# Optimization experiments

Hardware: AMD Instinct MI355X
Metric: run time of the kernel (lower is better)

## Reference

```python
import jax, jax.numpy as jnp
import numpy as np

N = 50000       # nodes
E = 800000      # edges (before self-loops)
F_IN = 128
HID = 64
HEADS = 4
OUT_DIM = 128
N_CLS = 2
NG = 500        # num graphs
SLOPE = 0.2     # GATConv leaky_relu negative slope
EPS = 1e-5      # BatchNorm eps


def setup_inputs() -> dict:
    key = jax.random.key(0)
    ks = jax.random.split(key, 24)
    s = 0.05
    d = {
        "x": jax.random.normal(ks[0], (N, F_IN), jnp.float32),
        "edge_index": jax.random.randint(ks[1], (2, E), 0, N, jnp.int64),
        "batch": jnp.sort(jax.random.randint(ks[2], (N,), 0, NG, jnp.int64)),
        # GATConv 1
        "W1": jax.random.normal(ks[3], (F_IN, HEADS * HID), jnp.float32) * s,
        "att_src1": jax.random.normal(ks[4], (HEADS, HID), jnp.float32) * s,
        "att_dst1": jax.random.normal(ks[5], (HEADS, HID), jnp.float32) * s,
        "b1": jnp.zeros((HEADS * HID,), jnp.float32),
        # BN1 (eval mode)
        "g1": jnp.ones((HEADS * HID,), jnp.float32),
        "be1": jnp.zeros((HEADS * HID,), jnp.float32),
        "rm1": jnp.zeros((HEADS * HID,), jnp.float32),
        "rv1": jnp.ones((HEADS * HID,), jnp.float32),
        # GATConv 2
        "W2": jax.random.normal(ks[6], (HEADS * HID, HEADS * HID), jnp.float32) * s,
        "att_src2": jax.random.normal(ks[7], (HEADS, HID), jnp.float32) * s,
        "att_dst2": jax.random.normal(ks[8], (HEADS, HID), jnp.float32) * s,
        "b2": jnp.zeros((HEADS * HID,), jnp.float32),
        # BN2 (eval mode)
        "g2": jnp.ones((HEADS * HID,), jnp.float32),
        "be2": jnp.zeros((HEADS * HID,), jnp.float32),
        "rm2": jnp.zeros((HEADS * HID,), jnp.float32),
        "rv2": jnp.ones((HEADS * HID,), jnp.float32),
        # MLP head
        "lw1": jax.random.normal(ks[9], (HEADS * HID, OUT_DIM), jnp.float32) * s,
        "lb1": jnp.zeros((OUT_DIM,), jnp.float32),
        "lw2": jax.random.normal(ks[10], (OUT_DIM, N_CLS), jnp.float32) * s,
        "lb2": jnp.zeros((N_CLS,), jnp.float32),
    }
    return d


def _gat_conv(x, src, dst, W, a_src, a_dst, b):
    """PyG GATConv (concat heads, add_self_loops=True, eval -> no dropout)."""
    n = x.shape[0]
    h = (x @ W).reshape(n, HEADS, -1)            # [N, H, C]
    loop = jnp.arange(n)
    s = jnp.concatenate([src, loop])             # self-loops appended
    d = jnp.concatenate([dst, loop])
    a_s = jnp.sum(h * a_src, axis=-1)            # [N, H]
    a_d = jnp.sum(h * a_dst, axis=-1)            # [N, H]
    e = jax.nn.leaky_relu(a_s[s] + a_d[d], SLOPE)   # [Et, H]
    # softmax over incoming edges per destination node
    m = jax.ops.segment_max(e, d, num_segments=n)
    ex = jnp.exp(e - m[d])
    denom = jax.ops.segment_sum(ex, d, num_segments=n)
    alpha = ex / denom[d]                        # [Et, H]
    msg = h[s] * alpha[:, :, None]               # [Et, H, C]
    out = jax.ops.segment_sum(msg, d, num_segments=n)
    return out.reshape(n, -1) + b


def _bn_eval(x, g, be, rm, rv):
    return (x - rm) * jax.lax.rsqrt(rv + EPS) * g + be


def reference(x, edge_index, batch, W1, att_src1, att_dst1, b1, g1, be1, rm1, rv1,
              W2, att_src2, att_dst2, b2, g2, be2, rm2, rv2, lw1, lb1, lw2, lb2):
    src, dst = edge_index[0], edge_index[1]
    h = jax.nn.relu(_gat_conv(x, src, dst, W1, att_src1, att_dst1, b1))
    h = _bn_eval(h, g1, be1, rm1, rv1)
    h = jax.nn.relu(_gat_conv(h, src, dst, W2, att_src2, att_dst2, b2))
    h = _bn_eval(h, g2, be2, rm2, rv2)
    # global mean pool over graphs
    sums = jax.ops.segment_sum(h, batch, num_segments=NG)
    cnt = jax.ops.segment_sum(jnp.ones((h.shape[0],), h.dtype), batch, num_segments=NG)
    pooled = sums / jnp.clip(cnt, 1.0)[:, None]
    z = jax.nn.relu(pooled @ lw1 + lb1)
    return z @ lw2 + lb2
```

## Files before the change

### kernel.cpp

```cpp
#include <hip/hip_runtime.h>
#include <hip/hip_bf16.h>
#include <math.h>

#define N_NODES 50000
#define M_PAD   50048
#define TILE_M  64
#define NBLK_GEMM (M_PAD / TILE_M)
#define N_EDGES 800000
#define F_IN 128
#define HID 64
#define HEADS 4
#define FEAT 256
#define OUT_DIM 128
#define N_CLS 2
#define NG 500
#define SLOPE 0.2f
#define BN_EPS 1e-5f
#define ECAP 64
#define ET (N_EDGES + N_NODES)
#define EH ((ET + 1) / 2)
#define NBLK_BUILD ((EH + 255) / 256)

#define XCONV (N_NODES * F_IN / 8)
#define XPAD_ULL ((M_PAD - N_NODES) * F_IN / 4)
#define HPAD_ULL ((M_PAD - N_NODES) * FEAT / 4)
#define PREP_THREADS (XCONV + F_IN * 256 + FEAT * 256 + XPAD_ULL + HPAD_ULL)
#define NBLK_PREP ((PREP_THREADS + 255) / 256)

typedef __attribute__((ext_vector_type(8))) short short8;
typedef __attribute__((ext_vector_type(4))) float floatx4;
typedef __attribute__((ext_vector_type(2))) float floatx2;

__device__ inline unsigned short f2bf(float f) {
    unsigned int u = __float_as_uint(f);
    unsigned int lsb = (u >> 16) & 1u;
    return (unsigned short)((u + 0x7fffu + lsb) >> 16);
}

__global__ __launch_bounds__(256) void prep_build(
    const float* __restrict__ x, const float* __restrict__ W1,
    const float* __restrict__ W2,
    unsigned short* __restrict__ xbf, unsigned short* __restrict__ W1T,
    unsigned short* __restrict__ W2T, unsigned short* __restrict__ h1bf,
    const int* __restrict__ src, const int* __restrict__ dst,
    int* __restrict__ deg, unsigned short* __restrict__ ell,
    int* __restrict__ ovf_cnt, int* __restrict__ ovf) {
    int b = blockIdx.x;
    int t = threadIdx.x;
    if (b < NBLK_PREP) {
        int gid = b * 256 + t;
        if (gid < XCONV) {
            const float4* xp = (const float4*)&x[gid * 8];
            float4 f0 = xp[0], f1 = xp[1];
            uint4 pk;
            pk.x = (unsigned)f2bf(f0.x) | ((unsigned)f2bf(f0.y) << 16);
            pk.y = (unsigned)f2bf(f0.z) | ((unsigned)f2bf(f0.w) << 16);
            pk.z = (unsigned)f2bf(f1.x) | ((unsigned)f2bf(f1.y) << 16);
            pk.w = (unsigned)f2bf(f1.z) | ((unsigned)f2bf(f1.w) << 16);
            *(uint4*)&xbf[gid * 8] = pk;
            return;
        }
        int j = gid - XCONV;
        if (j < F_IN * 256) {
            int k = j >> 8, n = j & 255;
            W1T[n * F_IN + k] = f2bf(W1[j]);
            return;
        }
        j -= F_IN * 256;
        if (j < FEAT * 256) {
            int k = j >> 8, n = j & 255;
            W2T[n * FEAT + k] = f2bf(W2[j]);
            return;
        }
        j -= FEAT * 256;
        if (j < XPAD_ULL) {
            ((unsigned long long*)(xbf + (size_t)N_NODES * F_IN))[j] = 0ULL;
            return;
        }
        j -= XPAD_ULL;
        if (j < HPAD_ULL) {
            ((unsigned long long*)(h1bf + (size_t)N_NODES * FEAT))[j] = 0ULL;
        }
        return;
    }
    int i = (b - NBLK_PREP) * 256 + t;
    if (i >= EH) return;
    int ss[2], dd[2], pp[2];
    int nv = 0;
    #pragma unroll
    for (int j = 0; j < 2; j++) {
        int e = i + j * EH;
        if (e < ET) {
            if (e < N_EDGES) { ss[nv] = src[e]; dd[nv] = dst[e]; }
            else             { ss[nv] = dd[nv] = e - N_EDGES; }
            nv++;
        }
    }
    #pragma unroll
    for (int j = 0; j < 2; j++)
        if (j < nv) pp[j] = atomicAdd(&deg[dd[j]], 1);
    #pragma unroll
    for (int j = 0; j < 2; j++) {
        if (j >= nv) continue;
        if (pp[j] < ECAP) {
            ell[dd[j] * ECAP + pp[j]] = (unsigned short)ss[j];
        } else {
            int k = atomicAdd(ovf_cnt, 1);
            ovf[2 * k] = ss[j];
            ovf[2 * k + 1] = dd[j];
        }
    }
}

template<int K>
__global__ __launch_bounds__(256, 4) void gemm_mfma(
    const unsigned short* __restrict__ Ab, const unsigned short* __restrict__ BT,
    const float* __restrict__ att_src, const float* __restrict__ att_dst,
    unsigned char* __restrict__ h8, float* __restrict__ a_s,
    float* __restrict__ a_d) {
    constexpr int LS = 40;
    constexpr int C8 = 272;
    __shared__ __align__(16) unsigned char smem_raw[(TILE_M + FEAT) * LS * 2];
    int t = threadIdx.x;

    unsigned short* As = (unsigned short*)smem_raw;
    unsigned short* Bs = As + TILE_M * LS;
    unsigned char*  s8 = smem_raw;
    int lane = t & 63, w = t >> 6;
    int row0 = blockIdx.x * TILE_M;
    int mrow = lane & 15, quad = lane >> 4;

    floatx4 acc[4][4] = {};

    int rA = t >> 2, cA = (t & 3) * 8;

    for (int k0 = 0; k0 < K; k0 += 32) {
        *(uint4*)&As[rA * LS + cA] =
            *(const uint4*)&Ab[(long long)(row0 + rA) * K + k0 + cA];
        #pragma unroll
        for (int j = 0; j < 4; j++) {
            int r = rA + j * 64;
            *(uint4*)&Bs[r * LS + cA] = *(const uint4*)&BT[(long long)r * K + k0 + cA];
        }
        __syncthreads();
        short8 bf[4];
        #pragma unroll
        for (int ni = 0; ni < 4; ni++)
            bf[ni] = *(const short8*)&Bs[(w * 64 + ni * 16 + mrow) * LS + quad * 8];
        #pragma unroll
        for (int mi = 0; mi < 4; mi++) {
            short8 af = *(const short8*)&As[(mi * 16 + mrow) * LS + quad * 8];
            #pragma unroll
            for (int ni = 0; ni < 4; ni++)
                acc[mi][ni] = __builtin_amdgcn_mfma_f32_16x16x32_bf16(af, bf[ni],
                                                                      acc[mi][ni], 0, 0, 0);
        }
        __syncthreads();
    }

    float ats[4], atd[4];
    #pragma unroll
    for (int ni = 0; ni < 4; ni++) {
        ats[ni] = att_src[w * 64 + ni * 16 + mrow];
        atd[ni] = att_dst[w * 64 + ni * 16 + mrow];
    }
    #pragma unroll
    for (int mi = 0; mi < 4; mi++) {
        #pragma unroll
        for (int r = 0; r < 4; r++) {
            int row = row0 + mi * 16 + quad * 4 + r;
            float ps = 0.f, pd = 0.f;
            #pragma unroll
            for (int ni = 0; ni < 4; ni++) {
                float v = acc[mi][ni][r];
                ps += v * ats[ni];
                pd += v * atd[ni];
            }
            #pragma unroll
            for (int off = 1; off < 16; off <<= 1) {
                ps += __shfl_xor(ps, off);
                pd += __shfl_xor(pd, off);
            }
            if (mrow == 0 && row < N_NODES) {
                a_s[row * 4 + w] = ps;
                a_d[row * 4 + w] = pd;
            }
        }
    }

    #pragma unroll
    for (int mi = 0; mi < 4; mi++)
        #pragma unroll
        for (int r = 0; r < 4; r++) {
            int row = mi * 16 + quad * 4 + r;
            #pragma unroll
            for (int ni = 0; ni < 4; ni += 2) {
                int pk = __builtin_amdgcn_cvt_pk_fp8_f32(acc[mi][ni][r],
                                                         acc[mi][ni + 1][r], 0, false);
                s8[row * C8 + w * 64 + ni * 16 + mrow]       = (unsigned char)(pk & 0xff);
                s8[row * C8 + w * 64 + (ni + 1) * 16 + mrow] = (unsigned char)((pk >> 8) & 0xff);
            }
        }
    __syncthreads();
    {
        int r2 = t >> 2, q = t & 3;
        const uint4* sp = (const uint4*)&s8[r2 * C8 + q * 64];
        uint4* dp = (uint4*)&h8[(long long)(row0 + r2) * FEAT + q * 64];
        #pragma unroll
        for (int k = 0; k < 4; k++)
            dp[k] = sp[k];
    }
}

__global__ __launch_bounds__(256) void gat_fused(
    const int* __restrict__ deg_arr, const unsigned short* __restrict__ ell,
    const int* __restrict__ ovf_cnt, const int* __restrict__ ovf,
    const float* __restrict__ a_s, const float* __restrict__ a_d,
    const unsigned char* __restrict__ h8, const float* __restrict__ bias,
    const float* __restrict__ g, const float* __restrict__ be,
    const float* __restrict__ rm, const float* __restrict__ rv,
    unsigned short* __restrict__ out16) {
    int t = threadIdx.x;
    int lane = t & 63;
    int w = t >> 6;
    int hd = lane >> 4;
    int d = blockIdx.x * 4 + w;

    __shared__ float p_lds[4 * ECAP * 4];
    __shared__ int   o_lds[4 * ECAP];
    float* pw = &p_lds[w * ECAP * 4];
    int*   ow = &o_lds[w * ECAP];

    const unsigned int* __restrict__ H1 = (const unsigned int*)h8;

    int deg = deg_arr[d];
    float4 ad4 = *(const float4*)&a_d[d * 4];

    float den = 0.f;
    float4 acc = make_float4(0.f, 0.f, 0.f, 0.f);

    if (deg <= ECAP) {
        float lg[4] = {-INFINITY, -INFINITY, -INFINITY, -INFINITY};
        if (lane < deg) {
            int s = ell[d * ECAP + lane];
            ow[lane] = s * 64;
            float4 as4 = *(const float4*)&a_s[s * 4];
            float e0 = as4.x + ad4.x; lg[0] = e0 > 0.f ? e0 : SLOPE * e0;
            float e1 = as4.y + ad4.y; lg[1] = e1 > 0.f ? e1 : SLOPE * e1;
            float e2 = as4.z + ad4.z; lg[2] = e2 > 0.f ? e2 : SLOPE * e2;
            float e3 = as4.w + ad4.w; lg[3] = e3 > 0.f ? e3 : SLOPE * e3;
        }
        float mm = fmaxf(fmaxf(lg[0], lg[1]), fmaxf(lg[2], lg[3]));
        #pragma unroll
        for (int off = 1; off < 64; off <<= 1) mm = fmaxf(mm, __shfl_xor(mm, off));
        if (lane < deg) {
            float4 pq;
            pq.x = __expf(lg[0] - mm);
            pq.y = __expf(lg[1] - mm);
            pq.z = __expf(lg[2] - mm);
            pq.w = __expf(lg[3] - mm);
            *(float4*)&pw[lane * 4] = pq;
        }
        int e = 0;
        for (; e + 1 < deg; e += 2) {
            int oA = ow[e], oB = ow[e + 1];
            float pA = pw[e * 4 + hd], pB = pw[(e + 1) * 4 + hd];
            int uA = (int)H1[oA + lane];
            int uB = (int)H1[oB + lane];
            den += pA + pB;
            floatx2 a0 = __builtin_amdgcn_cvt_pk_f32_fp8(uA, false);
            floatx2 a1 = __builtin_amdgcn_cvt_pk_f32_fp8(uA, true);
            floatx2 b0 = __builtin_amdgcn_cvt_pk_f32_fp8(uB, false);
            floatx2 b1 = __builtin_amdgcn_cvt_pk_f32_fp8(uB, true);
            acc.x += pA * a0.x; acc.y += pA * a0.y;
            acc.z += pA * a1.x; acc.w += pA * a1.y;
            acc.x += pB * b0.x; acc.y += pB * b0.y;
            acc.z += pB * b1.x; acc.w += pB * b1.y;
        }
        if (e < deg) {
            int oA = ow[e];
            float pA = pw[e * 4 + hd];
            int uA = (int)H1[oA + lane];
            den += pA;
            floatx2 a0 = __builtin_amdgcn_cvt_pk_f32_fp8(uA, false);
            floatx2 a1 = __builtin_amdgcn_cvt_pk_f32_fp8(uA, true);
            acc.x += pA * a0.x; acc.y += pA * a0.y;
            acc.z += pA * a1.x; acc.w += pA * a1.y;
        }
    } else {
        float m_old;
        {
            int s = ell[d * ECAP + lane];
            ow[lane] = s * 64;
            float4 as4 = *(const float4*)&a_s[s * 4];
            float lg[4];
            float e0 = as4.x + ad4.x; lg[0] = e0 > 0.f ? e0 : SLOPE * e0;
            float e1 = as4.y + ad4.y; lg[1] = e1 > 0.f ? e1 : SLOPE * e1;
            float e2 = as4.z + ad4.z; lg[2] = e2 > 0.f ? e2 : SLOPE * e2;
            float e3 = as4.w + ad4.w; lg[3] = e3 > 0.f ? e3 : SLOPE * e3;
            float mm = fmaxf(fmaxf(lg[0], lg[1]), fmaxf(lg[2], lg[3]));
            #pragma unroll
            for (int off = 1; off < 64; off <<= 1) mm = fmaxf(mm, __shfl_xor(mm, off));
            m_old = mm;
            float4 pq;
            pq.x = __expf(lg[0] - mm);
            pq.y = __expf(lg[1] - mm);
            pq.z = __expf(lg[2] - mm);
            pq.w = __expf(lg[3] - mm);
            *(float4*)&pw[lane * 4] = pq;
            for (int e = 0; e < ECAP; e++) {
                int oA = ow[e];
                float pA = pw[e * 4 + hd];
                int uA = (int)H1[oA + lane];
                den += pA;
                floatx2 a0 = __builtin_amdgcn_cvt_pk_f32_fp8(uA, false);
                floatx2 a1 = __builtin_amdgcn_cvt_pk_f32_fp8(uA, true);
                acc.x += pA * a0.x; acc.y += pA * a0.y;
                acc.z += pA * a1.x; acc.w += pA * a1.y;
            }
        }
        int nov = *ovf_cnt;
        for (int i = 0; i < nov; i++) {
            int s2 = ovf[2 * i], d2 = ovf[2 * i + 1];
            if (d2 != d) continue;
            float4 as4 = *(const float4*)&a_s[s2 * 4];
            float lg[4];
            float e0 = as4.x + ad4.x; lg[0] = e0 > 0.f ? e0 : SLOPE * e0;
            float e1 = as4.y + ad4.y; lg[1] = e1 > 0.f ? e1 : SLOPE * e1;
            float e2 = as4.z + ad4.z; lg[2] = e2 > 0.f ? e2 : SLOPE * e2;
            float e3 = as4.w + ad4.w; lg[3] = e3 > 0.f ? e3 : SLOPE * e3;
            float mmax = fmaxf(fmaxf(lg[0], lg[1]), fmaxf(lg[2], lg[3]));
            float m_new = fmaxf(m_old, mmax);
            float alpha = __expf(m_old - m_new);
            m_old = m_new;
            float ph = __expf(lg[hd] - m_new);
            acc.x *= alpha; acc.y *= alpha; acc.z *= alpha; acc.w *= alpha;
            den = den * alpha + ph;
            int u = (int)H1[s2 * 64 + lane];
            floatx2 a0 = __builtin_amdgcn_cvt_pk_f32_fp8(u, false);
            floatx2 a1 = __builtin_amdgcn_cvt_pk_f32_fp8(u, true);
            acc.x += ph * a0.x; acc.y += ph * a0.y;
            acc.z += ph * a1.x; acc.w += ph * a1.y;
        }
    }
    float inv = 1.f / den;
    int c0 = lane * 4;
    float4 bi = *(const float4*)&bias[c0];
    float4 gg = *(const float4*)&g[c0];
    float4 bb = *(const float4*)&be[c0];
    float4 mm4 = *(const float4*)&rm[c0];
    float4 vv = *(const float4*)&rv[c0];
    float v0 = fmaxf(acc.x * inv + bi.x, 0.f);
    float v1 = fmaxf(acc.y * inv + bi.y, 0.f);
    float v2 = fmaxf(acc.z * inv + bi.z, 0.f);
    float v3 = fmaxf(acc.w * inv + bi.w, 0.f);
    v0 = (v0 - mm4.x) * rsqrtf(vv.x + BN_EPS) * gg.x + bb.x;
    v1 = (v1 - mm4.y) * rsqrtf(vv.y + BN_EPS) * gg.y + bb.y;
    v2 = (v2 - mm4.z) * rsqrtf(vv.z + BN_EPS) * gg.z + bb.z;
    v3 = (v3 - mm4.w) * rsqrtf(vv.w + BN_EPS) * gg.w + bb.w;
    unsigned long long o =
        (unsigned long long)f2bf(v0) |
        ((unsigned long long)f2bf(v1) << 16) |
        ((unsigned long long)f2bf(v2) << 32) |
        ((unsigned long long)f2bf(v3) << 48);
    __builtin_nontemporal_store(o, (unsigned long long*)&out16[(long long)d * FEAT + c0]);
}

__global__ __launch_bounds__(256) void head_fused(
    const unsigned short* __restrict__ h2, const int* __restrict__ batch,
    const float* __restrict__ lw1, const float* __restrict__ lb1,
    const float* __restrict__ lw2, const float* __restrict__ lb2,
    float* __restrict__ out) {
    int gph = blockIdx.x;
    int t = threadIdx.x;
    __shared__ float pooled[FEAT];
    __shared__ float zl[OUT_DIM];
    __shared__ int lo_s, hi_s;
    if (t == 0) {
        int lo = 0, hi = N_NODES;
        while (lo < hi) { int mid = (lo + hi) >> 1; if (batch[mid] < gph) lo = mid + 1; else hi = mid; }
        lo_s = lo;
        int lo2 = 0, hi2 = N_NODES;
        while (lo2 < hi2) { int mid = (lo2 + hi2) >> 1; if (batch[mid] < gph + 1) lo2 = mid + 1; else hi2 = mid; }
        hi_s = lo2;
    }
    __syncthreads();
    int lo = lo_s, hi = hi_s;
    float a0 = 0.f, a1 = 0.f, a2 = 0.f, a3 = 0.f;
    int n = lo;
    for (; n + 3 < hi; n += 4) {
        a0 += __uint_as_float((unsigned)h2[(long long)n * FEAT + t] << 16);
        a1 += __uint_as_float((unsigned)h2[(long long)(n + 1) * FEAT + t] << 16);
        a2 += __uint_as_float((unsigned)h2[(long long)(n + 2) * FEAT + t] << 16);
        a3 += __uint_as_float((unsigned)h2[(long long)(n + 3) * FEAT + t] << 16);
    }
    for (; n < hi; n++) a0 += __uint_as_float((unsigned)h2[(long long)n * FEAT + t] << 16);
    float cnt = fmaxf((float)(hi - lo), 1.f);
    pooled[t] = (a0 + a1 + a2 + a3) / cnt;
    __syncthreads();
    int j = t >> 1, kh = t & 1;
    float zp = 0.f;
    #pragma unroll 8
    for (int k = kh * 128; k < kh * 128 + 128; k++)
        zp += pooled[k] * lw1[k * OUT_DIM + j];
    zp += __shfl_xor(zp, 1);
    if (kh == 0) zl[j] = fmaxf(zp + lb1[j], 0.f);
    __syncthreads();
    int w = t >> 6, lane = t & 63;
    if (w < 2) {
        float p = zl[lane] * lw2[lane * 2 + w] + zl[lane + 64] * lw2[(lane + 64) * 2 + w];
        #pragma unroll
        for (int off = 1; off < 64; off <<= 1) p += __shfl_xor(p, off);
        if (lane == 0) out[gph * 2 + w] = p + lb2[w];
    }
}

extern "C" void kernel_launch(void* const* d_in, const int* in_sizes, int n_in,
                              void* d_out, int out_size, void* d_ws, size_t ws_size,
                              hipStream_t stream) {
    const float* x       = (const float*)d_in[0];
    const int*   ei      = (const int*)d_in[1];
    const int*   batch   = (const int*)d_in[2];
    const float* W1      = (const float*)d_in[3];
    const float* att_s1  = (const float*)d_in[4];
    const float* att_d1  = (const float*)d_in[5];
    const float* b1      = (const float*)d_in[6];
    const float* g1      = (const float*)d_in[7];
    const float* be1     = (const float*)d_in[8];
    const float* rm1     = (const float*)d_in[9];
    const float* rv1     = (const float*)d_in[10];
    const float* W2      = (const float*)d_in[11];
    const float* att_s2  = (const float*)d_in[12];
    const float* att_d2  = (const float*)d_in[13];
    const float* b2      = (const float*)d_in[14];
    const float* g2      = (const float*)d_in[15];
    const float* be2     = (const float*)d_in[16];
    const float* rm2     = (const float*)d_in[17];
    const float* rv2     = (const float*)d_in[18];
    const float* lw1     = (const float*)d_in[19];
    const float* lb1     = (const float*)d_in[20];
    const float* lw2     = (const float*)d_in[21];
    const float* lb2     = (const float*)d_in[22];
    float* out           = (float*)d_out;

    const int* src = ei;
    const int* dst = ei + N_EDGES;

    char* p = (char*)d_ws;
    auto carve = [&p](size_t bytes) -> void* {
        void* r = (void*)p;
        p += (bytes + 63) & ~(size_t)63;
        return r;
    };
    unsigned short* h2bf = (unsigned short*)carve(sizeof(short) * (size_t)N_NODES * FEAT);
    float* a_s    = (float*)carve(sizeof(float) * N_NODES * HEADS);
    float* a_d    = (float*)carve(sizeof(float) * N_NODES * HEADS);
    int*   deg    = (int*)carve(sizeof(int) * N_NODES);
    int*   ovf_cnt= (int*)carve(sizeof(int) * 16);
    unsigned short* ell = (unsigned short*)carve(sizeof(short) * (size_t)N_NODES * ECAP);
    int*   ovf    = (int*)carve(sizeof(int) * 2 * ET);
    unsigned char*  h8   = (unsigned char*)carve((size_t)M_PAD * FEAT);
    unsigned short* xbf  = (unsigned short*)carve(sizeof(short) * (size_t)M_PAD * F_IN);
    unsigned short* h1bf = (unsigned short*)carve(sizeof(short) * (size_t)M_PAD * FEAT);
    unsigned short* w1t  = (unsigned short*)carve(sizeof(short) * FEAT * F_IN);
    unsigned short* w2t  = (unsigned short*)carve(sizeof(short) * FEAT * FEAT);

    hipMemsetAsync(deg, 0, sizeof(int) * N_NODES + 64, stream);

    prep_build<<<NBLK_PREP + NBLK_BUILD, 256, 0, stream>>>(
        x, W1, W2, xbf, w1t, w2t, h1bf, src, dst, deg, ell, ovf_cnt, ovf);

    gemm_mfma<F_IN><<<NBLK_GEMM, 256, 0, stream>>>(
        xbf, w1t, att_s1, att_d1, h8, a_s, a_d);
    gat_fused<<<N_NODES / 4, 256, 0, stream>>>(deg, ell, ovf_cnt, ovf, a_s, a_d, h8,
                                               b1, g1, be1, rm1, rv1, h1bf);

    gemm_mfma<FEAT><<<NBLK_GEMM, 256, 0, stream>>>(
        h1bf, w2t, att_s2, att_d2, h8, a_s, a_d);
    gat_fused<<<N_NODES / 4, 256, 0, stream>>>(deg, ell, ovf_cnt, ovf, a_s, a_d, h8,
                                               b2, g2, be2, rm2, rv2, h2bf);

    head_fused<<<NG, 256, 0, stream>>>(h2bf, batch, lw1, lb1, lw2, lb2, out);
}
```

Baseline: 311.8 us.

## Move edge adjacency build into first GEMM launch and init self-loops in prep

```diff
diff --git a/kernel.cpp b/kernel.cpp
--- a/kernel.cpp
+++ b/kernel.cpp
@@ -7,6 +7,8 @@
 #define TILE_M  64
 #define NBLK_GEMM (M_PAD / TILE_M)
 #define N_EDGES 800000
+#define EHALF   (N_EDGES / 2)
+#define NBLK_BUILD ((EHALF + 255) / 256)
 #define F_IN 128
 #define HID 64
 #define HEADS 4
@@ -17,14 +19,13 @@
 #define SLOPE 0.2f
 #define BN_EPS 1e-5f
 #define ECAP 64
-#define ET (N_EDGES + N_NODES)
-#define EH ((ET + 1) / 2)
-#define NBLK_BUILD ((EH + 255) / 256)
 
 #define XCONV (N_NODES * F_IN / 8)
+#define T_W1  (F_IN * 256)
+#define T_W2  (FEAT * 256)
 #define XPAD_ULL ((M_PAD - N_NODES) * F_IN / 4)
 #define HPAD_ULL ((M_PAD - N_NODES) * FEAT / 4)
-#define PREP_THREADS (XCONV + F_IN * 256 + FEAT * 256 + XPAD_ULL + HPAD_ULL)
+#define PREP_THREADS (XCONV + T_W1 + T_W2 + XPAD_ULL + HPAD_ULL + N_NODES)
 #define NBLK_PREP ((PREP_THREADS + 255) / 256)
 
 typedef __attribute__((ext_vector_type(8))) short short8;
@@ -37,97 +38,97 @@
     return (unsigned short)((u + 0x7fffu + lsb) >> 16);
 }
 
-__global__ __launch_bounds__(256) void prep_build(
+__global__ __launch_bounds__(256) void prep(
     const float* __restrict__ x, const float* __restrict__ W1,
     const float* __restrict__ W2,
     unsigned short* __restrict__ xbf, unsigned short* __restrict__ W1T,
     unsigned short* __restrict__ W2T, unsigned short* __restrict__ h1bf,
-    const int* __restrict__ src, const int* __restrict__ dst,
     int* __restrict__ deg, unsigned short* __restrict__ ell,
-    int* __restrict__ ovf_cnt, int* __restrict__ ovf) {
-    int b = blockIdx.x;
-    int t = threadIdx.x;
-    if (b < NBLK_PREP) {
-        int gid = b * 256 + t;
-        if (gid < XCONV) {
-            const float4* xp = (const float4*)&x[gid * 8];
-            float4 f0 = xp[0], f1 = xp[1];
-            uint4 pk;
-            pk.x = (unsigned)f2bf(f0.x) | ((unsigned)f2bf(f0.y) << 16);
-            pk.y = (unsigned)f2bf(f0.z) | ((unsigned)f2bf(f0.w) << 16);
-            pk.z = (unsigned)f2bf(f1.x) | ((unsigned)f2bf(f1.y) << 16);
-            pk.w = (unsigned)f2bf(f1.z) | ((unsigned)f2bf(f1.w) << 16);
-            *(uint4*)&xbf[gid * 8] = pk;
-            return;
-        }
-        int j = gid - XCONV;
-        if (j < F_IN * 256) {
-            int k = j >> 8, n = j & 255;
-            W1T[n * F_IN + k] = f2bf(W1[j]);
-            return;
-        }
-        j -= F_IN * 256;
-        if (j < FEAT * 256) {
-            int k = j >> 8, n = j & 255;
-            W2T[n * FEAT + k] = f2bf(W2[j]);
-            return;
-        }
-        j -= FEAT * 256;
-        if (j < XPAD_ULL) {
-            ((unsigned long long*)(xbf + (size_t)N_NODES * F_IN))[j] = 0ULL;
-            return;
-        }
-        j -= XPAD_ULL;
-        if (j < HPAD_ULL) {
-            ((unsigned long long*)(h1bf + (size_t)N_NODES * FEAT))[j] = 0ULL;
-        }
-        return;
-    }
-    int i = (b - NBLK_PREP) * 256 + t;
-    if (i >= EH) return;
-    int ss[2], dd[2], pp[2];
-    int nv = 0;
-    #pragma unroll
-    for (int j = 0; j < 2; j++) {
-        int e = i + j * EH;
-        if (e < ET) {
-            if (e < N_EDGES) { ss[nv] = src[e]; dd[nv] = dst[e]; }
-            else             { ss[nv] = dd[nv] = e - N_EDGES; }
-            nv++;
-        }
-    }
-    #pragma unroll
-    for (int j = 0; j < 2; j++)
-        if (j < nv) pp[j] = atomicAdd(&deg[dd[j]], 1);
-    #pragma unroll
-    for (int j = 0; j < 2; j++) {
-        if (j >= nv) continue;
-        if (pp[j] < ECAP) {
-            ell[dd[j] * ECAP + pp[j]] = (unsigned short)ss[j];
-        } else {
-            int k = atomicAdd(ovf_cnt, 1);
-            ovf[2 * k] = ss[j];
-            ovf[2 * k + 1] = dd[j];
-        }
-    }
-}
-
-template<int K>
+    int* __restrict__ ovf_cnt) {
+    int gid = blockIdx.x * 256 + threadIdx.x;
+    if (gid < XCONV) {
+        const float4* xp = (const float4*)&x[gid * 8];
+        float4 f0 = xp[0], f1 = xp[1];
+        uint4 pk;
+        pk.x = (unsigned)f2bf(f0.x) | ((unsigned)f2bf(f0.y) << 16);
+        pk.y = (unsigned)f2bf(f0.z) | ((unsigned)f2bf(f0.w) << 16);
+        pk.z = (unsigned)f2bf(f1.x) | ((unsigned)f2bf(f1.y) << 16);
+        pk.w = (unsigned)f2bf(f1.z) | ((unsigned)f2bf(f1.w) << 16);
+        *(uint4*)&xbf[gid * 8] = pk;
+        return;
+    }
+    int j = gid - XCONV;
+    if (j < T_W1) {
+        int k = j >> 8, n = j & 255;
+        W1T[n * F_IN + k] = f2bf(W1[j]);
+        return;
+    }
+    j -= T_W1;
+    if (j < T_W2) {
+        int k = j >> 8, n = j & 255;
+        W2T[n * FEAT + k] = f2bf(W2[j]);
+        return;
+    }
+    j -= T_W2;
+    if (j < XPAD_ULL) {
+        ((unsigned long long*)(xbf + (size_t)N_NODES * F_IN))[j] = 0ULL;
+        return;
+    }
+    j -= XPAD_ULL;
+    if (j < HPAD_ULL) {
+        ((unsigned long long*)(h1bf + (size_t)N_NODES * FEAT))[j] = 0ULL;
+        return;
+    }
+    j -= HPAD_ULL;
+    if (j < N_NODES) {
+        deg[j] = 1;
+        ell[(size_t)j * ECAP] = (unsigned short)j;
+        if (j == 0) *ovf_cnt = 0;
+    }
+}
+
+template<int K, bool BUILD>
 __global__ __launch_bounds__(256, 4) void gemm_mfma(
     const unsigned short* __restrict__ Ab, const unsigned short* __restrict__ BT,
     const float* __restrict__ att_src, const float* __restrict__ att_dst,
     unsigned char* __restrict__ h8, float* __restrict__ a_s,
-    float* __restrict__ a_d) {
+    float* __restrict__ a_d,
+    const int* __restrict__ src, const int* __restrict__ dst,
+    int* __restrict__ deg, unsigned short* __restrict__ ell,
+    int* __restrict__ ovf_cnt, int* __restrict__ ovf) {
     constexpr int LS = 40;
     constexpr int C8 = 272;
     __shared__ __align__(16) unsigned char smem_raw[(TILE_M + FEAT) * LS * 2];
     int t = threadIdx.x;
 
+    if (BUILD && blockIdx.x < NBLK_BUILD) {
+        int i = blockIdx.x * 256 + t;
+        if (i >= EHALF) return;
+        int s0 = src[i],          d0 = dst[i];
+        int s1 = src[i + EHALF],  d1 = dst[i + EHALF];
+        int p0 = atomicAdd(&deg[d0], 1);
+        int p1 = atomicAdd(&deg[d1], 1);
+        if (p0 < ECAP) {
+            ell[(size_t)d0 * ECAP + p0] = (unsigned short)s0;
+        } else {
+            int k = atomicAdd(ovf_cnt, 1);
+            ovf[2 * k] = s0; ovf[2 * k + 1] = d0;
+        }
+        if (p1 < ECAP) {
+            ell[(size_t)d1 * ECAP + p1] = (unsigned short)s1;
+        } else {
+            int k = atomicAdd(ovf_cnt, 1);
+            ovf[2 * k] = s1; ovf[2 * k + 1] = d1;
+        }
+        return;
+    }
+
+    int bid = BUILD ? (int)blockIdx.x - NBLK_BUILD : (int)blockIdx.x;
     unsigned short* As = (unsigned short*)smem_raw;
     unsigned short* Bs = As + TILE_M * LS;
     unsigned char*  s8 = smem_raw;
     int lane = t & 63, w = t >> 6;
-    int row0 = blockIdx.x * TILE_M;
+    int row0 = bid * TILE_M;
     int mrow = lane & 15, quad = lane >> 4;
 
     floatx4 acc[4][4] = {};
@@ -242,7 +243,7 @@
     if (deg <= ECAP) {
         float lg[4] = {-INFINITY, -INFINITY, -INFINITY, -INFINITY};
         if (lane < deg) {
-            int s = ell[d * ECAP + lane];
+            int s = ell[(size_t)d * ECAP + lane];
             ow[lane] = s * 64;
             float4 as4 = *(const float4*)&a_s[s * 4];
             float e0 = as4.x + ad4.x; lg[0] = e0 > 0.f ? e0 : SLOPE * e0;
@@ -290,7 +291,7 @@
     } else {
         float m_old;
         {
-            int s = ell[d * ECAP + lane];
+            int s = ell[(size_t)d * ECAP + lane];
             ow[lane] = s * 64;
             float4 as4 = *(const float4*)&a_s[s * 4];
             float lg[4];
@@ -458,25 +459,25 @@
     int*   deg    = (int*)carve(sizeof(int) * N_NODES);
     int*   ovf_cnt= (int*)carve(sizeof(int) * 16);
     unsigned short* ell = (unsigned short*)carve(sizeof(short) * (size_t)N_NODES * ECAP);
-    int*   ovf    = (int*)carve(sizeof(int) * 2 * ET);
+    int*   ovf    = (int*)carve(sizeof(int) * 2 * (N_EDGES + N_NODES));
     unsigned char*  h8   = (unsigned char*)carve((size_t)M_PAD * FEAT);
     unsigned short* xbf  = (unsigned short*)carve(sizeof(short) * (size_t)M_PAD * F_IN);
     unsigned short* h1bf = (unsigned short*)carve(sizeof(short) * (size_t)M_PAD * FEAT);
     unsigned short* w1t  = (unsigned short*)carve(sizeof(short) * FEAT * F_IN);
     unsigned short* w2t  = (unsigned short*)carve(sizeof(short) * FEAT * FEAT);
 
-    hipMemsetAsync(deg, 0, sizeof(int) * N_NODES + 64, stream);
-
-    prep_build<<<NBLK_PREP + NBLK_BUILD, 256, 0, stream>>>(
-        x, W1, W2, xbf, w1t, w2t, h1bf, src, dst, deg, ell, ovf_cnt, ovf);
-
-    gemm_mfma<F_IN><<<NBLK_GEMM, 256, 0, stream>>>(
-        xbf, w1t, att_s1, att_d1, h8, a_s, a_d);
+    prep<<<NBLK_PREP, 256, 0, stream>>>(
+        x, W1, W2, xbf, w1t, w2t, h1bf, deg, ell, ovf_cnt);
+
+    gemm_mfma<F_IN, true><<<NBLK_BUILD + NBLK_GEMM, 256, 0, stream>>>(
+        xbf, w1t, att_s1, att_d1, h8, a_s, a_d,
+        src, dst, deg, ell, ovf_cnt, ovf);
     gat_fused<<<N_NODES / 4, 256, 0, stream>>>(deg, ell, ovf_cnt, ovf, a_s, a_d, h8,
                                                b1, g1, be1, rm1, rv1, h1bf);
 
-    gemm_mfma<FEAT><<<NBLK_GEMM, 256, 0, stream>>>(
-        h1bf, w2t, att_s2, att_d2, h8, a_s, a_d);
+    gemm_mfma<FEAT, false><<<NBLK_GEMM, 256, 0, stream>>>(
+        h1bf, w2t, att_s2, att_d2, h8, a_s, a_d,
+        nullptr, nullptr, nullptr, nullptr, nullptr, nullptr);
     gat_fused<<<N_NODES / 4, 256, 0, stream>>>(deg, ell, ovf_cnt, ovf, a_s, a_d, h8,
                                                b2, g2, be2, rm2, rv2, h2bf);
 
```

Result: no change. 309.9 us (-0.6%).
